# Kernel tuning notes

Measured on AMD Instinct MI355X. Metric: run time of the kernel, lower is better.

The kernel has to match this reference:

```python
import jax, jax.numpy as jnp
import numpy as np

D_MIN, D_MAX, D_COUNT = 0.0, 6.0, 16
HIDDEN = 128
N_NODES, N_EDGES = 50000, 1600000


def _rbf(D):
    # D: [E] -> [E, D_COUNT]
    mu = jnp.linspace(D_MIN, D_MAX, D_COUNT, dtype=D.dtype)  # [16]
    sigma = (D_MAX - D_MIN) / D_COUNT
    return jnp.exp(-(((D[:, None] - mu[None, :]) / sigma) ** 2))


def setup_inputs() -> dict:
    key = jax.random.key(0)
    k1, k2, k3, k4 = jax.random.split(key, 4)
    pos = jax.random.normal(k1, (N_NODES, 3), dtype=jnp.float32) * 3.0
    edge_index = jax.random.randint(k2, (2, N_EDGES), 0, N_NODES, dtype=jnp.int64)
    # Linear(16, hidden): PyTorch default init U(-1/sqrt(16), 1/sqrt(16))
    bound = 1.0 / np.sqrt(D_COUNT)
    W = jax.random.uniform(k3, (D_COUNT, HIDDEN), jnp.float32, -bound, bound)
    b = jax.random.uniform(k4, (HIDDEN,), jnp.float32, -bound, bound)
    return {"pos": pos, "edge_index": edge_index, "W": W, "b": b}


def reference(pos, edge_index, W, b):
    # gather endpoints: [E, 3]
    coord_diff = pos[edge_index[0]] - pos[edge_index[1]]
    dist = jnp.linalg.norm(coord_diff, axis=1)        # [E]
    rbf = _rbf(dist)                                  # [E, 16]
    return jax.nn.sigmoid(rbf @ W + b)                # [E, hidden]
```

## Files before the change

### kernel.cpp

```cpp
#include <hip/hip_runtime.h>
#include <math.h>

#define N_NODES 50000
#define N_EDGES 1600000
#define HIDDEN  128
#define DC      16
#define EPB     128
#define BLOCK   256
#define RBF_LD  20

#define MU_STEP   0.4f
#define INV_SIGMA 2.6666666666666665f

typedef float f32x2 __attribute__((ext_vector_type(2)));
typedef float f32x4 __attribute__((ext_vector_type(4)));
typedef f32x4 f32x4u __attribute__((aligned(4)));

__device__ __forceinline__ float fast_sigmoid(float x) {
    float e = __expf(-x);
    return __builtin_amdgcn_rcpf(1.0f + e);
}

__device__ __forceinline__ f32x2 fma2(float s, f32x2 w, f32x2 a) {
    a.x = fmaf(s, w.x, a.x);
    a.y = fmaf(s, w.y, a.y);
    return a;
}

__global__ __launch_bounds__(BLOCK, 6) void edge_attr_kernel(
    const float* __restrict__ pos,
    const int* __restrict__ ei,
    const float* __restrict__ W,
    const float* __restrict__ b,
    float* __restrict__ out)
{
    __shared__ float dist_s[EPB];
    __shared__ float rbf_s[EPB][RBF_LD];

    const int tid = threadIdx.x;
    const int h2  = tid & 63;
    const int wv  = tid >> 6;

    f32x2 wcol[DC];
    #pragma unroll
    for (int k = 0; k < DC; ++k)
        wcol[k] = *reinterpret_cast<const f32x2*>(W + k * HIDDEN + h2 * 2);
    const f32x2 bias = *reinterpret_cast<const f32x2*>(b + h2 * 2);

    const long row0 = (long)blockIdx.x * EPB;

    if (tid < EPB) {
        const int e = (int)row0 + tid;
        const int s = ei[e];
        const int d = ei[N_EDGES + e];
        const f32x4 ps = *reinterpret_cast<const f32x4u*>(pos + 3 * s);
        const f32x4 pd = *reinterpret_cast<const f32x4u*>(pos + 3 * d);
        const float dx = ps.x - pd.x;
        const float dy = ps.y - pd.y;
        const float dz = ps.z - pd.z;
        dist_s[tid] = sqrtf(dx * dx + dy * dy + dz * dz);
    }
    __syncthreads();

    {
        const int el = tid & 127;
        const int kg = tid >> 7;
        const float dist = dist_s[el];
        f32x4 r0, r1;
        #pragma unroll
        for (int j = 0; j < 4; ++j) {
            const float t = (dist - MU_STEP * (float)(kg * 8 + j)) * INV_SIGMA;
            r0[j] = __expf(-t * t);
        }
        #pragma unroll
        for (int j = 0; j < 4; ++j) {
            const float t = (dist - MU_STEP * (float)(kg * 8 + 4 + j)) * INV_SIGMA;
            r1[j] = __expf(-t * t);
        }
        *reinterpret_cast<f32x4*>(&rbf_s[el][kg * 8 + 0]) = r0;
        *reinterpret_cast<f32x4*>(&rbf_s[el][kg * 8 + 4]) = r1;
    }
    __syncthreads();

    float* op = out + (row0 + wv) * HIDDEN + h2 * 2;
    #pragma unroll 4
    for (int i = 0; i < EPB / 4; ++i) {
        const int el = wv + i * 4;

        const f32x4* rp = reinterpret_cast<const f32x4*>(&rbf_s[el][0]);
        const f32x4 ra = rp[0];
        const f32x4 rb = rp[1];
        const f32x4 rc = rp[2];
        const f32x4 rd = rp[3];

        f32x2 acc = bias;
        acc = fma2(ra.x, wcol[0],  acc);
        acc = fma2(ra.y, wcol[1],  acc);
        acc = fma2(ra.z, wcol[2],  acc);
        acc = fma2(ra.w, wcol[3],  acc);
        acc = fma2(rb.x, wcol[4],  acc);
        acc = fma2(rb.y, wcol[5],  acc);
        acc = fma2(rb.z, wcol[6],  acc);
        acc = fma2(rb.w, wcol[7],  acc);
        acc = fma2(rc.x, wcol[8],  acc);
        acc = fma2(rc.y, wcol[9],  acc);
        acc = fma2(rc.z, wcol[10], acc);
        acc = fma2(rc.w, wcol[11], acc);
        acc = fma2(rd.x, wcol[12], acc);
        acc = fma2(rd.y, wcol[13], acc);
        acc = fma2(rd.z, wcol[14], acc);
        acc = fma2(rd.w, wcol[15], acc);

        f32x2 res;
        res.x = fast_sigmoid(acc.x);
        res.y = fast_sigmoid(acc.y);

        __builtin_nontemporal_store(res, reinterpret_cast<f32x2*>(op));
        op += 4 * HIDDEN;
    }
}

extern "C" void kernel_launch(void* const* d_in, const int* in_sizes, int n_in,
                              void* d_out, int out_size, void* d_ws, size_t ws_size,
                              hipStream_t stream) {
    const float* pos = (const float*)d_in[0];
    const int*   ei  = (const int*)d_in[1];
    const float* W   = (const float*)d_in[2];
    const float* b   = (const float*)d_in[3];
    float*       out = (float*)d_out;

    dim3 grid(N_EDGES / EPB);
    edge_attr_kernel<<<grid, BLOCK, 0, stream>>>(pos, ei, W, b, out);
}
```

Measured before the change: 824.3 us.

## Make blocks persistent over five tiles with double-buffered prefetch of next tile's RBF

Each block now handles five 128-edge tiles instead of one, loading the next tile's indices and positions while the current tile's matmul and sigmoid run, with the RBF staged in a double-buffered shared array. The goal is to hide gather latency behind the output-write phase and to reuse the per-thread weight registers across tiles. The FMA is rewritten as a vector elementwise FMA so the compiler can emit packed FMA, and the output stores switch from nontemporal to normal stores. The grid shrinks to 2500 blocks, so there is less parallelism to hide latency, and the normal stores may pollute the cache.

```diff
diff --git a/kernel.cpp b/kernel.cpp
--- a/kernel.cpp
+++ b/kernel.cpp
@@ -7,6 +7,8 @@
 #define DC      16
 #define EPB     128
 #define BLOCK   256
+#define TILES   5
+#define GRID    2500
 #define RBF_LD  20
 
 #define MU_STEP   0.4f
@@ -21,10 +23,9 @@
     return __builtin_amdgcn_rcpf(1.0f + e);
 }
 
-__device__ __forceinline__ f32x2 fma2(float s, f32x2 w, f32x2 a) {
-    a.x = fmaf(s, w.x, a.x);
-    a.y = fmaf(s, w.y, a.y);
-    return a;
+__device__ __forceinline__ f32x2 fma2v(float s, f32x2 w, f32x2 a) {
+    f32x2 sv = s;
+    return __builtin_elementwise_fma(sv, w, a);
 }
 
 __global__ __launch_bounds__(BLOCK, 6) void edge_attr_kernel(
@@ -34,12 +35,15 @@
     const float* __restrict__ b,
     float* __restrict__ out)
 {
-    __shared__ float dist_s[EPB];
-    __shared__ float rbf_s[EPB][RBF_LD];
+    __shared__ float rbf_s[2][EPB][RBF_LD];
 
     const int tid = threadIdx.x;
     const int h2  = tid & 63;
     const int wv  = tid >> 6;
+    const int el  = tid & 127;
+    const int kg  = tid >> 7;
+
+    const long eb = (long)blockIdx.x * (TILES * EPB);
 
     f32x2 wcol[DC];
     #pragma unroll
@@ -47,76 +51,94 @@
         wcol[k] = *reinterpret_cast<const f32x2*>(W + k * HIDDEN + h2 * 2);
     const f32x2 bias = *reinterpret_cast<const f32x2*>(b + h2 * 2);
 
-    const long row0 = (long)blockIdx.x * EPB;
-
-    if (tid < EPB) {
-        const int e = (int)row0 + tid;
+    {
+        const long e = eb + el;
         const int s = ei[e];
         const int d = ei[N_EDGES + e];
         const f32x4 ps = *reinterpret_cast<const f32x4u*>(pos + 3 * s);
         const f32x4 pd = *reinterpret_cast<const f32x4u*>(pos + 3 * d);
-        const float dx = ps.x - pd.x;
-        const float dy = ps.y - pd.y;
-        const float dz = ps.z - pd.z;
-        dist_s[tid] = sqrtf(dx * dx + dy * dy + dz * dz);
+        const float dx = ps.x - pd.x, dy = ps.y - pd.y, dz = ps.z - pd.z;
+        const float dist = sqrtf(dx * dx + dy * dy + dz * dz);
+        f32x4 r0, r1;
+        #pragma unroll
+        for (int j = 0; j < 4; ++j) {
+            const float t0 = (dist - MU_STEP * (float)(kg * 8 + j)) * INV_SIGMA;
+            const float t1 = (dist - MU_STEP * (float)(kg * 8 + 4 + j)) * INV_SIGMA;
+            r0[j] = __expf(-t0 * t0);
+            r1[j] = __expf(-t1 * t1);
+        }
+        *reinterpret_cast<f32x4*>(&rbf_s[0][el][kg * 8 + 0]) = r0;
+        *reinterpret_cast<f32x4*>(&rbf_s[0][el][kg * 8 + 4]) = r1;
     }
     __syncthreads();
 
-    {
-        const int el = tid & 127;
-        const int kg = tid >> 7;
-        const float dist = dist_s[el];
-        f32x4 r0, r1;
-        #pragma unroll
-        for (int j = 0; j < 4; ++j) {
-            const float t = (dist - MU_STEP * (float)(kg * 8 + j)) * INV_SIGMA;
-            r0[j] = __expf(-t * t);
+    #pragma unroll 1
+    for (int t = 0; t < TILES; ++t) {
+        const int cur = t & 1;
+
+        f32x4 psn = {}, pdn = {};
+        if (t + 1 < TILES) {
+            const long e = eb + (long)(t + 1) * EPB + el;
+            const int sn = ei[e];
+            const int dn = ei[N_EDGES + e];
+            psn = *reinterpret_cast<const f32x4u*>(pos + 3 * sn);
+            pdn = *reinterpret_cast<const f32x4u*>(pos + 3 * dn);
         }
-        #pragma unroll
-        for (int j = 0; j < 4; ++j) {
-            const float t = (dist - MU_STEP * (float)(kg * 8 + 4 + j)) * INV_SIGMA;
-            r1[j] = __expf(-t * t);
+
+        const long row0 = eb + (long)t * EPB;
+        float* op = out + (row0 + wv) * HIDDEN + h2 * 2;
+        #pragma unroll 4
+        for (int i = 0; i < EPB / 4; ++i) {
+            const int erow = wv + i * 4;
+
+            const f32x4* rp = reinterpret_cast<const f32x4*>(&rbf_s[cur][erow][0]);
+            const f32x4 ra = rp[0];
+            const f32x4 rb = rp[1];
+            const f32x4 rc = rp[2];
+            const f32x4 rd = rp[3];
+
+            f32x2 acc = bias;
+            acc = fma2v(ra.x, wcol[0],  acc);
+            acc = fma2v(ra.y, wcol[1],  acc);
+            acc = fma2v(ra.z, wcol[2],  acc);
+            acc = fma2v(ra.w, wcol[3],  acc);
+            acc = fma2v(rb.x, wcol[4],  acc);
+            acc = fma2v(rb.y, wcol[5],  acc);
+            acc = fma2v(rb.z, wcol[6],  acc);
+            acc = fma2v(rb.w, wcol[7],  acc);
+            acc = fma2v(rc.x, wcol[8],  acc);
+            acc = fma2v(rc.y, wcol[9],  acc);
+            acc = fma2v(rc.z, wcol[10], acc);
+            acc = fma2v(rc.w, wcol[11], acc);
+            acc = fma2v(rd.x, wcol[12], acc);
+            acc = fma2v(rd.y, wcol[13], acc);
+            acc = fma2v(rd.z, wcol[14], acc);
+            acc = fma2v(rd.w, wcol[15], acc);
+
+            f32x2 res;
+            res.x = fast_sigmoid(acc.x);
+            res.y = fast_sigmoid(acc.y);
+
+            *reinterpret_cast<f32x2*>(op) = res;
+            op += 4 * HIDDEN;
         }
-        *reinterpret_cast<f32x4*>(&rbf_s[el][kg * 8 + 0]) = r0;
-        *reinterpret_cast<f32x4*>(&rbf_s[el][kg * 8 + 4]) = r1;
-    }
-    __syncthreads();
 
-    float* op = out + (row0 + wv) * HIDDEN + h2 * 2;
-    #pragma unroll 4
-    for (int i = 0; i < EPB / 4; ++i) {
-        const int el = wv + i * 4;
+        if (t + 1 < TILES) {
+            const float dx = psn.x - pdn.x, dy = psn.y - pdn.y, dz = psn.z - pdn.z;
+            const float dist = sqrtf(dx * dx + dy * dy + dz * dz);
+            f32x4 r0, r1;
+            #pragma unroll
+            for (int j = 0; j < 4; ++j) {
+                const float t0 = (dist - MU_STEP * (float)(kg * 8 + j)) * INV_SIGMA;
+                const float t1 = (dist - MU_STEP * (float)(kg * 8 + 4 + j)) * INV_SIGMA;
+                r0[j] = __expf(-t0 * t0);
+                r1[j] = __expf(-t1 * t1);
+            }
+            *reinterpret_cast<f32x4*>(&rbf_s[cur ^ 1][el][kg * 8 + 0]) = r0;
+            *reinterpret_cast<f32x4*>(&rbf_s[cur ^ 1][el][kg * 8 + 4]) = r1;
+        }
 
-        const f32x4* rp = reinterpret_cast<const f32x4*>(&rbf_s[el][0]);
-        const f32x4 ra = rp[0];
-        const f32x4 rb = rp[1];
-        const f32x4 rc = rp[2];
-        const f32x4 rd = rp[3];
-
-        f32x2 acc = bias;
-        acc = fma2(ra.x, wcol[0],  acc);
-        acc = fma2(ra.y, wcol[1],  acc);
-        acc = fma2(ra.z, wcol[2],  acc);
-        acc = fma2(ra.w, wcol[3],  acc);
-        acc = fma2(rb.x, wcol[4],  acc);
-        acc = fma2(rb.y, wcol[5],  acc);
-        acc = fma2(rb.z, wcol[6],  acc);
-        acc = fma2(rb.w, wcol[7],  acc);
-        acc = fma2(rc.x, wcol[8],  acc);
-        acc = fma2(rc.y, wcol[9],  acc);
-        acc = fma2(rc.z, wcol[10], acc);
-        acc = fma2(rc.w, wcol[11], acc);
-        acc = fma2(rd.x, wcol[12], acc);
-        acc = fma2(rd.y, wcol[13], acc);
-        acc = fma2(rd.z, wcol[14], acc);
-        acc = fma2(rd.w, wcol[15], acc);
-
-        f32x2 res;
-        res.x = fast_sigmoid(acc.x);
-        res.y = fast_sigmoid(acc.y);
-
-        __builtin_nontemporal_store(res, reinterpret_cast<f32x2*>(op));
-        op += 4 * HIDDEN;
+        __syncthreads();
     }
 }
 
@@ -129,6 +151,6 @@
     const float* b   = (const float*)d_in[3];
     float*       out = (float*)d_out;
 
-    dim3 grid(N_EDGES / EPB);
+    dim3 grid(GRID);
     edge_attr_kernel<<<grid, BLOCK, 0, stream>>>(pos, ei, W, b, out);
 }
```

New measurement: 841.7 us. 2.1% more time.
